# Performance work log

Hardware: AMD Instinct MI355X
Metric: run time of the kernel (lower is better)

The kernel has to match this reference:

```python
import jax, jax.numpy as jnp
import numpy as np

N = 128            # codeword length (power of 2)
LIST = 8           # SCL list size
L2 = 2 * LIST      # decoders kept during path expansion
STAGES = 7         # log2(N)
LLR_MAX = 30.0
BATCH = 2048
FROZEN_POS = np.arange(N // 2)
FROZEN_IND = np.zeros(N, dtype=bool)
FROZEN_IND[FROZEN_POS] = True
INFO_POS = np.setdiff1d(np.arange(N), FROZEN_POS)


def _cn_op(x, y):
    # min-sum boxplus with LLR clipping
    x = jnp.clip(x, -LLR_MAX, LLR_MAX)
    y = jnp.clip(y, -LLR_MAX, LLR_MAX)
    return jnp.sign(x) * jnp.sign(y) * jnp.minimum(jnp.abs(x), jnp.abs(y))


def _vn_op(x, y, u):
    return (1.0 - 2.0 * u) * x + y


def _leaf(state, i):
    # Update single bit i across all 2L decoders, update path metrics,
    # and for info bits sort + duplicate the best L paths.
    uhat, llr, pm, ptr, bidx = state
    frozen = bool(FROZEN_IND[i])
    if not frozen:
        # set bit=1 for the upper half of decoders (path expansion)
        u_slice = uhat[:, :, 0, i]
        u_slice = u_slice.at[bidx[:, None], ptr[:, LIST:]].set(1.0)
        uhat = uhat.at[:, :, 0, i].set(u_slice)
    # path metric update, Eq.(10) of Stimming et al.
    u = jnp.take_along_axis(uhat[:, :, 0, i], ptr, axis=1)
    l = jnp.clip(jnp.take_along_axis(llr[:, :, 0, i], ptr, axis=1), -LLR_MAX, LLR_MAX)
    pm = pm + jax.nn.softplus(-(1.0 - 2.0 * u) * l)
    if not frozen:
        order = jnp.argsort(pm, axis=-1)
        pm = jnp.take_along_axis(pm, order, axis=1)
        ptr = jnp.take_along_axis(ptr, order, axis=1)
        lo = ptr[:, :LIST]
        up = ptr[:, LIST:]
        uhat = uhat.at[bidx[:, None], up].set(uhat[bidx[:, None], lo])
        llr = llr.at[bidx[:, None], up].set(llr[bidx[:, None], lo])
        pm = pm.at[:, LIST:].set(pm[:, :LIST])
    return (uhat, llr, pm, ptr, bidx)


def _decode(state, start, length):
    # recursive SCL tree traversal over contiguous index block [start, start+length)
    if length == 1:
        return _leaf(state, start)
    s = int(np.log2(length))
    h = length // 2
    uhat, llr, pm, ptr, bidx = state
    lsl = slice(start, start + h)
    rsl = slice(start + h, start + length)
    # f (check-node) update -> left child
    f = _cn_op(llr[:, :, s, lsl], llr[:, :, s, rsl])
    llr = llr.at[:, :, s - 1, lsl].set(f)
    uhat, llr, pm, ptr, bidx = _decode((uhat, llr, pm, ptr, bidx), start, h)
    # g (variable-node) update -> right child
    g = _vn_op(llr[:, :, s, lsl], llr[:, :, s, rsl], uhat[:, :, s - 1, lsl])
    llr = llr.at[:, :, s - 1, rsl].set(g)
    uhat, llr, pm, ptr, bidx = _decode((uhat, llr, pm, ptr, bidx), start + h, h)
    # combine partial sums: left XOR right, right pass-through
    ul = uhat[:, :, s - 1, lsl]
    ur = uhat[:, :, s - 1, rsl]
    ux = ul + ur - 2.0 * ul * ur  # XOR for {0,1} values (differentiable form)
    uhat = uhat.at[:, :, s, start:start + length].set(jnp.concatenate([ux, ur], axis=-1))
    return (uhat, llr, pm, ptr, bidx)


def setup_inputs() -> dict:
    key = jax.random.key(0)
    inputs = 2.0 * jax.random.normal(key, (BATCH, N), dtype=jnp.float32)
    return {"inputs": inputs}


def reference(inputs):
    bs = inputs.shape[0]
    llr_ch = -inputs.astype(jnp.float32)  # logits -> LLR sign convention
    uhat = jnp.zeros((bs, L2, STAGES + 1, N), jnp.float32)
    llr = jnp.zeros((bs, L2, STAGES + 1, N), jnp.float32)
    llr = llr.at[:, :, STAGES, :].set(llr_ch[:, None, :])
    pm = jnp.zeros((bs, L2), jnp.float32)
    pm = pm.at[:, 1:LIST].set(LLR_MAX).at[:, LIST + 1:].set(LLR_MAX)
    ptr = jnp.tile(jnp.arange(L2)[None, :], (bs, 1))
    bidx = jnp.arange(bs)
    uhat, llr, pm, ptr, _ = _decode((uhat, llr, pm, ptr, bidx), 0, N)
    # final sort and de-permutation of the list dimension
    order = jnp.argsort(pm, axis=-1)
    pm = jnp.take_along_axis(pm, order, axis=1)
    ptr = jnp.take_along_axis(ptr, order, axis=1)
    uhat = uhat[bidx[:, None], ptr]
    cand = jnp.argmin(pm, axis=-1)
    c_hat = uhat[bidx, cand, 0, :]       # [bs, n] best codeword estimate
    return c_hat[:, INFO_POS]            # [bs, k] info bits
```

## Files before the change

### kernel.cpp

```cpp
#include <hip/hip_runtime.h>
#include <math.h>

#define LMAX 30.0f
typedef unsigned long long ull;
typedef unsigned int u32;

__device__ __forceinline__ float clip30(float x) { return fminf(fmaxf(x, -LMAX), LMAX); }
__device__ __forceinline__ float cnop(float x, float y) {
    x = clip30(x); y = clip30(y);
    const float m = fminf(fabsf(x), fabsf(y));
    const unsigned sg = (__float_as_uint(x) ^ __float_as_uint(y)) & 0x80000000u;
    return __uint_as_float(__float_as_uint(m) | sg);
}

#define SWZI(x, PAT) __builtin_amdgcn_ds_swizzle((x), (PAT))
#define SWZF(x, PAT) __int_as_float(__builtin_amdgcn_ds_swizzle(__float_as_int(x), (PAT)))

template<int CTRL>
__device__ __forceinline__ int dppi(int x) {
    return __builtin_amdgcn_update_dpp(x, x, CTRL, 0xF, 0xF, false);
}
template<int CTRL>
__device__ __forceinline__ float dppf(float x) {
    return __int_as_float(dppi<CTRL>(__float_as_int(x)));
}
#define CTL_XOR8 0x128
#define CTL_XOR2 0x4E
#define CTL_XOR1 0xB1

#if __has_builtin(__builtin_amdgcn_permlane16_swap)
typedef int v2j_ __attribute__((ext_vector_type(2)));
__device__ __forceinline__ int swap16i(int x) {
    v2j_ r = __builtin_amdgcn_permlane16_swap(x, x, false, false);
    return (r[0] != x) ? r[0] : r[1];
}
#else
__device__ __forceinline__ int swap16i(int x) { return SWZI(x, 0x401F); }
#endif
__device__ __forceinline__ float swap16f(float x) { return __int_as_float(swap16i(__float_as_int(x))); }

__device__ __forceinline__ float gfb(float v, int a) {
    return __int_as_float(__builtin_amdgcn_ds_bpermute(a, __float_as_int(v)));
}
__device__ __forceinline__ u32 gub(u32 v, int a) {
    return (u32)__builtin_amdgcn_ds_bpermute(a, (int)v);
}

template<int LO>
__device__ __forceinline__ u32 gbits(u32 lo, u32 hi) {
    if constexpr (LO >= 32) return hi >> (LO - 32);
    else if constexpr (LO == 0) return lo;
    else return (lo >> LO) | (hi << (32 - LO));
}

__device__ __forceinline__ u32 enc2(u32 w)  { w ^= (w >> 1) & 0x1u; return w; }
__device__ __forceinline__ u32 enc4(u32 w)  { w ^= (w >> 1) & 0x5u; w ^= (w >> 2) & 0x3u; return w; }
__device__ __forceinline__ u32 enc8(u32 w)  { w ^= (w >> 1) & 0x55u; w ^= (w >> 2) & 0x33u;
                                              w ^= (w >> 4) & 0x0fu; return w; }
__device__ __forceinline__ u32 enc16(u32 w) { w ^= (w >> 1) & 0x5555u; w ^= (w >> 2) & 0x3333u;
                                              w ^= (w >> 4) & 0x0f0fu; w ^= (w >> 8) & 0x00ffu; return w; }
__device__ __forceinline__ u32 enc32(u32 w) { w ^= (w >> 1) & 0x55555555u; w ^= (w >> 2) & 0x33333333u;
                                              w ^= (w >> 4) & 0x0f0f0f0fu; w ^= (w >> 8) & 0x00ff00ffu;
                                              w ^= (w >> 16) & 0x0000ffffu; return w; }

struct Dec {
    float C[32];
    float S5[16], S4[8], S3[4], R2[4], R1[2];
    float pm;
    u32 uhLo, uhHi;
    int rF;
    int q, pos, gbase, A0, idx0;
    u32 upB;
    bool isUp;
};

__device__ __forceinline__ void f6(Dec& s) {
    #pragma unroll
    for (int k = 0; k < 16; ++k) s.S5[k] = cnop(s.C[k], s.C[k + 16]);
}
template<int II> __device__ __forceinline__ void g6(Dec& s) {
    const u32 ub = enc32(gbits<II - 96>(s.uhLo, s.uhHi));
    #pragma unroll
    for (int k = 0; k < 16; ++k) {
        const int u = (ub >> (s.q + 2 * k)) & 1;
        s.S5[k] = u ? (s.C[k + 16] - s.C[k]) : (s.C[k + 16] + s.C[k]);
    }
}
__device__ __forceinline__ void f5(Dec& s) {
    #pragma unroll
    for (int k = 0; k < 8; ++k) s.S4[k] = cnop(s.S5[k], s.S5[k + 8]);
}
template<int II> __device__ __forceinline__ void g5(Dec& s) {
    const u32 ub = enc16(gbits<II - 80>(s.uhLo, s.uhHi) & 0xffffu);
    #pragma unroll
    for (int k = 0; k < 8; ++k) {
        const int u = (ub >> (s.q + 2 * k)) & 1;
        s.S4[k] = u ? (s.S5[k + 8] - s.S5[k]) : (s.S5[k + 8] + s.S5[k]);
    }
}
__device__ __forceinline__ void f4(Dec& s) {
    #pragma unroll
    for (int k = 0; k < 4; ++k) s.S3[k] = cnop(s.S4[k], s.S4[k + 4]);
}
template<int II> __device__ __forceinline__ void g4(Dec& s) {
    const u32 ub = enc8(gbits<II - 72>(s.uhLo, s.uhHi) & 0xffu);
    #pragma unroll
    for (int k = 0; k < 4; ++k) {
        const int u = (ub >> (s.q + 2 * k)) & 1;
        s.S3[k] = u ? (s.S4[k + 4] - s.S4[k]) : (s.S4[k + 4] + s.S4[k]);
    }
}
__device__ __forceinline__ void repl2(Dec& s, float t0, float t1) {
    const float P0 = swap16f(t0), P1 = swap16f(t1);
    s.R2[0] = s.q ? P0 : t0; s.R2[1] = s.q ? t0 : P0;
    s.R2[2] = s.q ? P1 : t1; s.R2[3] = s.q ? t1 : P1;
}
__device__ __forceinline__ void f3r(Dec& s) {
    repl2(s, cnop(s.S3[0], s.S3[2]), cnop(s.S3[1], s.S3[3]));
}
template<int II> __device__ __forceinline__ void g3r(Dec& s) {
    const u32 ub = enc4(gbits<II - 68>(s.uhLo, s.uhHi) & 0xfu);
    const int u0 = (ub >> s.q) & 1, u1 = (ub >> (s.q + 2)) & 1;
    repl2(s, u0 ? (s.S3[2] - s.S3[0]) : (s.S3[2] + s.S3[0]),
             u1 ? (s.S3[3] - s.S3[1]) : (s.S3[3] + s.S3[1]));
}
__device__ __forceinline__ void f2(Dec& s) {
    s.R1[0] = cnop(s.R2[0], s.R2[2]); s.R1[1] = cnop(s.R2[1], s.R2[3]);
}
template<int II> __device__ __forceinline__ void g2(Dec& s) {
    const u32 ub = enc2(gbits<II - 66>(s.uhLo, s.uhHi) & 3u);
    s.R1[0] = (ub & 1) ? (s.R2[2] - s.R2[0]) : (s.R2[2] + s.R2[0]);
    s.R1[1] = (ub & 2) ? (s.R2[3] - s.R2[1]) : (s.R2[3] + s.R2[1]);
}

template<int II, bool CLONE>
__device__ __forceinline__ void leaf(Dec& s, float l0) {
    if constexpr (II - 64 < 32) s.uhLo |= s.upB << (II - 64);
    else                        s.uhHi |= s.upB << (II - 96);
    const float l = clip30(l0);
    const float tail = log1pf(expf(-fabsf(l)));
    s.pm += (s.isUp ? fmaxf(l, 0.0f) : fmaxf(-l, 0.0f)) + tail;
    int r = 0;
    {
        const u32 pmB = __float_as_uint(s.pm);
        #pragma unroll
        for (int k = 0; k < 8; ++k) {
            const u32 pmj = gub((u32)__float_as_int(s.pm) * 0u + (u32)0, 0) * 0u;
        }
    }
    (void)r;
}

template<int II, bool CLONE>
__device__ __forceinline__ void leafR(Dec& s, float l0) {
    if constexpr (II - 64 < 32) s.uhLo |= s.upB << (II - 64);
    else                        s.uhHi |= s.upB << (II - 96);
    const float l = clip30(l0);
    const float tail = log1pf(expf(-fabsf(l)));
    s.pm += (s.isUp ? fmaxf(l, 0.0f) : fmaxf(-l, 0.0f)) + tail;
    int r = 0;
    {
        const u32 pmB = __float_as_uint(s.pm);
        #pragma unroll
        for (int k = 0; k < 8; ++k) {
            const u32 pmj = (u32)__builtin_amdgcn_ds_bpermute(s.A0 + 4 * k, __float_as_int(s.pm));
            r += ((pmj < pmB) || (pmj == pmB && (s.idx0 + k) < s.pos)) ? 1 : 0;
        }
    }
    r += swap16i(r);
    s.rF = r;
    if constexpr (CLONE) {
        const int inv = __builtin_amdgcn_ds_permute((r | s.gbase) << 2, s.pos);
        const int p8 = dppi<CTL_XOR8>(inv);
        const int ga = ((s.isUp ? p8 : inv) | s.gbase) << 2;
        s.pm = gfb(s.pm, ga);
        s.uhLo = gub(s.uhLo, ga);
        if constexpr (II >= 96) s.uhHi = gub(s.uhHi, ga);
        if constexpr ((((II) >> 0) & 1) == 0 && II >= 66) {
            s.R1[0] = gfb(s.R1[0], ga); s.R1[1] = gfb(s.R1[1], ga);
        }
        if constexpr ((((II) >> 1) & 1) == 0 && II >= 68) {
            #pragma unroll
            for (int e = 0; e < 4; ++e) s.R2[e] = gfb(s.R2[e], ga);
        }
        if constexpr ((((II) >> 2) & 1) == 0 && II >= 72) {
            #pragma unroll
            for (int e = 0; e < 4; ++e) s.S3[e] = gfb(s.S3[e], ga);
        }
        if constexpr ((((II) >> 3) & 1) == 0 && II >= 80) {
            #pragma unroll
            for (int e = 0; e < 8; ++e) s.S4[e] = gfb(s.S4[e], ga);
        }
        if constexpr ((((II) >> 4) & 1) == 0 && II >= 96) {
            #pragma unroll
            for (int e = 0; e < 16; ++e) s.S5[e] = gfb(s.S5[e], ga);
        }
    }
}

template<int II> __device__ __forceinline__ void evenLeaf(Dec& s) {
    constexpr int t = (II == 64) ? 6 : __builtin_ctz(II);
    if constexpr (t >= 6) f6(s);
    if constexpr (t == 5) g6<II>(s);
    if constexpr (t >= 5) f5(s);
    if constexpr (t == 4) g5<II>(s);
    if constexpr (t >= 4) f4(s);
    if constexpr (t == 3) g4<II>(s);
    if constexpr (t >= 3) f3r(s);
    if constexpr (t == 2) g3r<II>(s);
    if constexpr (t >= 2) f2(s);
    if constexpr (t == 1) g2<II>(s);
    const float l0 = cnop(s.R1[0], s.R1[1]);
    leafR<II, true>(s, l0);
}
template<int II> __device__ __forceinline__ void oddLeaf(Dec& s) {
    const int ug = (int)(gbits<II - 65>(s.uhLo, s.uhHi) & 1u);
    const float l0 = ug ? (s.R1[1] - s.R1[0]) : (s.R1[1] + s.R1[0]);
    leafR<II, (II != 127)>(s, l0);
}
template<int II> __device__ __forceinline__ void runPairs(Dec& s) {
    evenLeaf<II>(s);
    oddLeaf<II + 1>(s);
    if constexpr (II + 2 < 128) runPairs<II + 2>(s);
}

#define RLF(x, J) __uint_as_float((u32)__builtin_amdgcn_readlane(__float_as_int(x), (J)))

__global__ __launch_bounds__(64) void scl_kernel(const float* __restrict__ in,
                                                 float* __restrict__ out) {
    __shared__ float chS[128];
    const int lane = threadIdx.x;
    const int w = lane & 31;
    const int d = lane >> 5;
    const int dbase = lane & 32;

    Dec s;
    s.pos = lane & 15;
    s.q = (lane >> 4) & 1;
    s.gbase = lane & 48;
    s.isUp = (lane & 8) != 0;
    s.upB = (u32)((lane >> 3) & 1);
    s.idx0 = s.q << 3;
    s.A0 = (dbase | (s.q << 3)) << 2;
    s.uhLo = 0; s.uhHi = 0; s.rF = 0;

    const size_t base = ((size_t)blockIdx.x * 2 + d) * 128;
    const float a1 = -in[base + w],      c1 = -in[base + 64 + w];
    const float a2 = -in[base + 32 + w], c2 = -in[base + 96 + w];
    chS[d * 64 + w] = a1 + c1;
    chS[d * 64 + 32 + w] = a2 + c2;
    __syncthreads();
    #pragma unroll
    for (int k = 0; k < 32; ++k) s.C[k] = chS[d * 64 + s.q + 2 * k];

    float v1 = cnop(a1, c1), v2 = cnop(a2, c2);
    { const float n1 = cnop(v1, v2); v2 = v1 + v2; v1 = n1; }
    { const float o1 = swap16f(v1), o2 = swap16f(v2);
      v1 = (w & 16) ? (o1 + v1) : cnop(v1, o1);
      v2 = (w & 16) ? (o2 + v2) : cnop(v2, o2); }
    { const float o1 = dppf<CTL_XOR8>(v1), o2 = dppf<CTL_XOR8>(v2);
      v1 = (w & 8) ? (o1 + v1) : cnop(v1, o1);
      v2 = (w & 8) ? (o2 + v2) : cnop(v2, o2); }
    { const float o1 = SWZF(v1, 0x101F), o2 = SWZF(v2, 0x101F);
      v1 = (w & 4) ? (o1 + v1) : cnop(v1, o1);
      v2 = (w & 4) ? (o2 + v2) : cnop(v2, o2); }
    { const float o1 = dppf<CTL_XOR2>(v1), o2 = dppf<CTL_XOR2>(v2);
      v1 = (w & 2) ? (o1 + v1) : cnop(v1, o1);
      v2 = (w & 2) ? (o2 + v2) : cnop(v2, o2); }
    { const float o1 = dppf<CTL_XOR1>(v1), o2 = dppf<CTL_XOR1>(v2);
      v1 = (w & 1) ? (o1 + v1) : cnop(v1, o1);
      v2 = (w & 1) ? (o2 + v2) : cnop(v2, o2); }
    const float sp1 = fmaxf(-clip30(v1), 0.0f) + log1pf(expf(-fabsf(clip30(v1))));
    const float sp2 = fmaxf(-clip30(v2), 0.0f) + log1pf(expf(-fabsf(clip30(v2))));

    s.pm = ((s.pos == 0) || (s.pos == 8)) ? 0.0f : LMAX;
    if (lane < 32) {
        #pragma unroll
        for (int j = 0; j < 32; ++j) s.pm += RLF(sp1, j);
        #pragma unroll
        for (int j = 0; j < 32; ++j) s.pm += RLF(sp2, j);
    } else {
        #pragma unroll
        for (int j = 32; j < 64; ++j) s.pm += RLF(sp1, j);
        #pragma unroll
        for (int j = 32; j < 64; ++j) s.pm += RLF(sp2, j);
    }

    runPairs<64>(s);

    const ull m = __ballot(s.rF == 0);
    const int bl = dbase + (int)__builtin_ctz((u32)(m >> dbase));
    const u32 lo = gub(s.uhLo, bl << 2);
    const u32 hi = gub(s.uhHi, bl << 2);
    const ull uhB = ((ull)hi << 32) | lo;
    const size_t ob = ((size_t)blockIdx.x * 2 + d) * 64;
    out[ob + w] = (float)((uhB >> w) & 1ULL);
    out[ob + 32 + w] = (float)((uhB >> (w + 32)) & 1ULL);
}

extern "C" void kernel_launch(void* const* d_in, const int* in_sizes, int n_in,
                              void* d_out, int out_size, void* d_ws, size_t ws_size,
                              hipStream_t stream) {
    (void)n_in; (void)out_size; (void)d_ws; (void)ws_size;
    const float* in = (const float*)d_in[0];
    float* out = (float*)d_out;
    const int batch = in_sizes[0] / 128;
    scl_kernel<<<dim3(batch / 2), dim3(64), 0, stream>>>(in, out);
}
```

Baseline: 53.43 us.

## Fold the 64 info-bit leaves into a two-iteration loop over 32-bit halves

Replaces the fully unrolled traversal of all 64 info leaves with a non-unrolled loop over two halves of 32 leaves. Decoded bits are kept in a previous-half and current-half word instead of a lo/hi pair with compile-time bit offsets, and the g6 step reads the finished first half. The aim is to roughly halve code size and instruction-cache pressure. The cost is runtime checks on h and an extra permute of the previous-half word on every clone in the second half.

```diff
diff --git a/kernel.cpp b/kernel.cpp
--- a/kernel.cpp
+++ b/kernel.cpp
@@ -44,13 +44,6 @@
 }
 __device__ __forceinline__ u32 gub(u32 v, int a) {
     return (u32)__builtin_amdgcn_ds_bpermute(a, (int)v);
-}
-
-template<int LO>
-__device__ __forceinline__ u32 gbits(u32 lo, u32 hi) {
-    if constexpr (LO >= 32) return hi >> (LO - 32);
-    else if constexpr (LO == 0) return lo;
-    else return (lo >> LO) | (hi << (32 - LO));
 }
 
 __device__ __forceinline__ u32 enc2(u32 w)  { w ^= (w >> 1) & 0x1u; return w; }
@@ -67,7 +60,7 @@
     float C[32];
     float S5[16], S4[8], S3[4], R2[4], R1[2];
     float pm;
-    u32 uhLo, uhHi;
+    u32 uhPrev, uhCur;
     int rF;
     int q, pos, gbase, A0, idx0;
     u32 upB;
@@ -78,8 +71,8 @@
     #pragma unroll
     for (int k = 0; k < 16; ++k) s.S5[k] = cnop(s.C[k], s.C[k + 16]);
 }
-template<int II> __device__ __forceinline__ void g6(Dec& s) {
-    const u32 ub = enc32(gbits<II - 96>(s.uhLo, s.uhHi));
+__device__ __forceinline__ void g6p(Dec& s) {
+    const u32 ub = enc32(s.uhPrev);
     #pragma unroll
     for (int k = 0; k < 16; ++k) {
         const int u = (ub >> (s.q + 2 * k)) & 1;
@@ -90,8 +83,8 @@
     #pragma unroll
     for (int k = 0; k < 8; ++k) s.S4[k] = cnop(s.S5[k], s.S5[k + 8]);
 }
-template<int II> __device__ __forceinline__ void g5(Dec& s) {
-    const u32 ub = enc16(gbits<II - 80>(s.uhLo, s.uhHi) & 0xffffu);
+template<int L> __device__ __forceinline__ void g5l(Dec& s) {
+    const u32 ub = enc16((s.uhCur >> (L - 16)) & 0xffffu);
     #pragma unroll
     for (int k = 0; k < 8; ++k) {
         const int u = (ub >> (s.q + 2 * k)) & 1;
@@ -102,8 +95,8 @@
     #pragma unroll
     for (int k = 0; k < 4; ++k) s.S3[k] = cnop(s.S4[k], s.S4[k + 4]);
 }
-template<int II> __device__ __forceinline__ void g4(Dec& s) {
-    const u32 ub = enc8(gbits<II - 72>(s.uhLo, s.uhHi) & 0xffu);
+template<int L> __device__ __forceinline__ void g4l(Dec& s) {
+    const u32 ub = enc8((s.uhCur >> (L - 8)) & 0xffu);
     #pragma unroll
     for (int k = 0; k < 4; ++k) {
         const int u = (ub >> (s.q + 2 * k)) & 1;
@@ -118,8 +111,8 @@
 __device__ __forceinline__ void f3r(Dec& s) {
     repl2(s, cnop(s.S3[0], s.S3[2]), cnop(s.S3[1], s.S3[3]));
 }
-template<int II> __device__ __forceinline__ void g3r(Dec& s) {
-    const u32 ub = enc4(gbits<II - 68>(s.uhLo, s.uhHi) & 0xfu);
+template<int L> __device__ __forceinline__ void g3rl(Dec& s) {
+    const u32 ub = enc4((s.uhCur >> (L - 4)) & 0xfu);
     const int u0 = (ub >> s.q) & 1, u1 = (ub >> (s.q + 2)) & 1;
     repl2(s, u0 ? (s.S3[2] - s.S3[0]) : (s.S3[2] + s.S3[0]),
              u1 ? (s.S3[3] - s.S3[1]) : (s.S3[3] + s.S3[1]));
@@ -127,16 +120,15 @@
 __device__ __forceinline__ void f2(Dec& s) {
     s.R1[0] = cnop(s.R2[0], s.R2[2]); s.R1[1] = cnop(s.R2[1], s.R2[3]);
 }
-template<int II> __device__ __forceinline__ void g2(Dec& s) {
-    const u32 ub = enc2(gbits<II - 66>(s.uhLo, s.uhHi) & 3u);
+template<int L> __device__ __forceinline__ void g2l(Dec& s) {
+    const u32 ub = enc2((s.uhCur >> (L - 2)) & 3u);
     s.R1[0] = (ub & 1) ? (s.R2[2] - s.R2[0]) : (s.R2[2] + s.R2[0]);
     s.R1[1] = (ub & 2) ? (s.R2[3] - s.R2[1]) : (s.R2[3] + s.R2[1]);
 }
 
-template<int II, bool CLONE>
-__device__ __forceinline__ void leaf(Dec& s, float l0) {
-    if constexpr (II - 64 < 32) s.uhLo |= s.upB << (II - 64);
-    else                        s.uhHi |= s.upB << (II - 96);
+template<int L, int CLONEMODE>
+__device__ __forceinline__ void leafR(Dec& s, float l0, int h) {
+    s.uhCur |= s.upB << L;
     const float l = clip30(l0);
     const float tail = log1pf(expf(-fabsf(l)));
     s.pm += (s.isUp ? fmaxf(l, 0.0f) : fmaxf(-l, 0.0f)) + tail;
@@ -145,83 +137,64 @@
         const u32 pmB = __float_as_uint(s.pm);
         #pragma unroll
         for (int k = 0; k < 8; ++k) {
-            const u32 pmj = gub((u32)__float_as_int(s.pm) * 0u + (u32)0, 0) * 0u;
-        }
-    }
-    (void)r;
-}
-
-template<int II, bool CLONE>
-__device__ __forceinline__ void leafR(Dec& s, float l0) {
-    if constexpr (II - 64 < 32) s.uhLo |= s.upB << (II - 64);
-    else                        s.uhHi |= s.upB << (II - 96);
-    const float l = clip30(l0);
-    const float tail = log1pf(expf(-fabsf(l)));
-    s.pm += (s.isUp ? fmaxf(l, 0.0f) : fmaxf(-l, 0.0f)) + tail;
-    int r = 0;
-    {
-        const u32 pmB = __float_as_uint(s.pm);
-        #pragma unroll
-        for (int k = 0; k < 8; ++k) {
             const u32 pmj = (u32)__builtin_amdgcn_ds_bpermute(s.A0 + 4 * k, __float_as_int(s.pm));
             r += ((pmj < pmB) || (pmj == pmB && (s.idx0 + k) < s.pos)) ? 1 : 0;
         }
     }
     r += swap16i(r);
     s.rF = r;
-    if constexpr (CLONE) {
-        const int inv = __builtin_amdgcn_ds_permute((r | s.gbase) << 2, s.pos);
-        const int p8 = dppi<CTL_XOR8>(inv);
-        const int ga = ((s.isUp ? p8 : inv) | s.gbase) << 2;
-        s.pm = gfb(s.pm, ga);
-        s.uhLo = gub(s.uhLo, ga);
-        if constexpr (II >= 96) s.uhHi = gub(s.uhHi, ga);
-        if constexpr ((((II) >> 0) & 1) == 0 && II >= 66) {
-            s.R1[0] = gfb(s.R1[0], ga); s.R1[1] = gfb(s.R1[1], ga);
+    if constexpr (CLONEMODE != 0) {
+        if (CLONEMODE == 1 || h == 0) {
+            const int inv = __builtin_amdgcn_ds_permute((r | s.gbase) << 2, s.pos);
+            const int p8 = dppi<CTL_XOR8>(inv);
+            const int ga = ((s.isUp ? p8 : inv) | s.gbase) << 2;
+            s.pm = gfb(s.pm, ga);
+            s.uhCur = gub(s.uhCur, ga);
+            if (h != 0) s.uhPrev = gub(s.uhPrev, ga);
+            if constexpr ((L & 1) == 0) {
+                s.R1[0] = gfb(s.R1[0], ga); s.R1[1] = gfb(s.R1[1], ga);
+            }
+            if constexpr ((L & 2) == 0) {
+                #pragma unroll
+                for (int e = 0; e < 4; ++e) s.R2[e] = gfb(s.R2[e], ga);
+            }
+            if constexpr ((L & 4) == 0) {
+                #pragma unroll
+                for (int e = 0; e < 4; ++e) s.S3[e] = gfb(s.S3[e], ga);
+            }
+            if constexpr ((L & 8) == 0) {
+                #pragma unroll
+                for (int e = 0; e < 8; ++e) s.S4[e] = gfb(s.S4[e], ga);
+            }
+            if constexpr ((L & 16) == 0) {
+                #pragma unroll
+                for (int e = 0; e < 16; ++e) s.S5[e] = gfb(s.S5[e], ga);
+            }
         }
-        if constexpr ((((II) >> 1) & 1) == 0 && II >= 68) {
-            #pragma unroll
-            for (int e = 0; e < 4; ++e) s.R2[e] = gfb(s.R2[e], ga);
-        }
-        if constexpr ((((II) >> 2) & 1) == 0 && II >= 72) {
-            #pragma unroll
-            for (int e = 0; e < 4; ++e) s.S3[e] = gfb(s.S3[e], ga);
-        }
-        if constexpr ((((II) >> 3) & 1) == 0 && II >= 80) {
-            #pragma unroll
-            for (int e = 0; e < 8; ++e) s.S4[e] = gfb(s.S4[e], ga);
-        }
-        if constexpr ((((II) >> 4) & 1) == 0 && II >= 96) {
-            #pragma unroll
-            for (int e = 0; e < 16; ++e) s.S5[e] = gfb(s.S5[e], ga);
-        }
-    }
-}
-
-template<int II> __device__ __forceinline__ void evenLeaf(Dec& s) {
-    constexpr int t = (II == 64) ? 6 : __builtin_ctz(II);
-    if constexpr (t >= 6) f6(s);
-    if constexpr (t == 5) g6<II>(s);
-    if constexpr (t >= 5) f5(s);
-    if constexpr (t == 4) g5<II>(s);
+    }
+}
+
+template<int J> __device__ __forceinline__ void evenL(Dec& s, int h) {
+    constexpr int t = __builtin_ctz(J);
+    if constexpr (t == 4) g5l<J>(s);
     if constexpr (t >= 4) f4(s);
-    if constexpr (t == 3) g4<II>(s);
+    if constexpr (t == 3) g4l<J>(s);
     if constexpr (t >= 3) f3r(s);
-    if constexpr (t == 2) g3r<II>(s);
+    if constexpr (t == 2) g3rl<J>(s);
     if constexpr (t >= 2) f2(s);
-    if constexpr (t == 1) g2<II>(s);
+    if constexpr (t == 1) g2l<J>(s);
     const float l0 = cnop(s.R1[0], s.R1[1]);
-    leafR<II, true>(s, l0);
-}
-template<int II> __device__ __forceinline__ void oddLeaf(Dec& s) {
-    const int ug = (int)(gbits<II - 65>(s.uhLo, s.uhHi) & 1u);
+    leafR<J, 1>(s, l0, h);
+}
+template<int J> __device__ __forceinline__ void oddL(Dec& s, int h) {
+    const int ug = (int)((s.uhCur >> (J - 1)) & 1u);
     const float l0 = ug ? (s.R1[1] - s.R1[0]) : (s.R1[1] + s.R1[0]);
-    leafR<II, (II != 127)>(s, l0);
-}
-template<int II> __device__ __forceinline__ void runPairs(Dec& s) {
-    evenLeaf<II>(s);
-    oddLeaf<II + 1>(s);
-    if constexpr (II + 2 < 128) runPairs<II + 2>(s);
+    leafR<J, (J == 31 ? 2 : 1)>(s, l0, h);
+}
+template<int J> __device__ __forceinline__ void pairs(Dec& s, int h) {
+    evenL<J>(s, h);
+    oddL<J + 1>(s, h);
+    if constexpr (J + 2 <= 30) pairs<J + 2>(s, h);
 }
 
 #define RLF(x, J) __uint_as_float((u32)__builtin_amdgcn_readlane(__float_as_int(x), (J)))
@@ -242,7 +215,7 @@
     s.upB = (u32)((lane >> 3) & 1);
     s.idx0 = s.q << 3;
     s.A0 = (dbase | (s.q << 3)) << 2;
-    s.uhLo = 0; s.uhHi = 0; s.rF = 0;
+    s.uhPrev = 0; s.uhCur = 0; s.rF = 0;
 
     const size_t base = ((size_t)blockIdx.x * 2 + d) * 128;
     const float a1 = -in[base + w],      c1 = -in[base + 64 + w];
@@ -286,16 +259,23 @@
         for (int j = 32; j < 64; ++j) s.pm += RLF(sp2, j);
     }
 
-    runPairs<64>(s);
+    #pragma unroll 1
+    for (int h = 0; h < 2; ++h) {
+        if (h == 0) f6(s); else g6p(s);
+        f5(s); f4(s); f3r(s); f2(s);
+        { const float l0 = cnop(s.R1[0], s.R1[1]); leafR<0, 1>(s, l0, h); }
+        oddL<1>(s, h);
+        pairs<2>(s, h);
+        if (h == 0) { s.uhPrev = s.uhCur; s.uhCur = 0; }
+    }
 
     const ull m = __ballot(s.rF == 0);
     const int bl = dbase + (int)__builtin_ctz((u32)(m >> dbase));
-    const u32 lo = gub(s.uhLo, bl << 2);
-    const u32 hi = gub(s.uhHi, bl << 2);
-    const ull uhB = ((ull)hi << 32) | lo;
+    const u32 b0 = gub(s.uhPrev, bl << 2);
+    const u32 b1 = gub(s.uhCur, bl << 2);
     const size_t ob = ((size_t)blockIdx.x * 2 + d) * 64;
-    out[ob + w] = (float)((uhB >> w) & 1ULL);
-    out[ob + 32 + w] = (float)((uhB >> (w + 32)) & 1ULL);
+    out[ob + w] = (float)((b0 >> w) & 1u);
+    out[ob + 32 + w] = (float)((b1 >> w) & 1u);
 }
 
 extern "C" void kernel_launch(void* const* d_in, const int* in_sizes, int n_in,
```

Result: no change. 52.90 us (-1.0%).
